# Optimization experiments

Hardware: AMD Instinct MI355X
Metric: run time of the kernel (lower is better)

Reference implementation:

```python
import math
import jax, jax.numpy as jnp
import numpy as np

NUM_HEADS = 8
FACTOR = 5


def setup_inputs() -> dict:
    key = jax.random.key(0)
    ks = jax.random.split(key, 8)
    B, N, C = 8, 4096, 512
    s = 0.02
    x = jax.random.normal(ks[0], (B, N, C), dtype=jnp.float32)
    Wq = jax.random.normal(ks[1], (C, C), dtype=jnp.float32) * s
    Wk = jax.random.normal(ks[2], (C, C), dtype=jnp.float32) * s
    Wv = jax.random.normal(ks[3], (C, C), dtype=jnp.float32) * s
    Wp = jax.random.normal(ks[4], (C, C), dtype=jnp.float32) * s
    bq = jnp.zeros((C,), jnp.float32)
    bk = jnp.zeros((C,), jnp.float32)
    bv = jnp.zeros((C,), jnp.float32)
    bp = jnp.zeros((C,), jnp.float32)
    sample_k = min(FACTOR * int(np.ceil(np.log(N))), N)  # 45
    index_sample = jax.random.randint(ks[5], (N, sample_k), 0, N, dtype=jnp.int64)
    return {"x": x, "Wq": Wq, "bq": bq, "Wk": Wk, "bk": bk,
            "Wv": Wv, "bv": bv, "Wp": Wp, "bp": bp,
            "index_sample": index_sample}


def reference(x, Wq, bq, Wk, bk, Wv, bv, Wp, bp, index_sample):
    B, N, C = x.shape
    H = NUM_HEADS
    Dh = C // H
    L_Q = L_K = N
    # qkv projections (torch Linear: x @ W.T + b; W sampled symmetric so use x @ W + b)
    q = (x @ Wq + bq).reshape(B, N, H, Dh).transpose(0, 2, 1, 3)  # [B,H,L,Dh]
    k = (x @ Wk + bk).reshape(B, N, H, Dh).transpose(0, 2, 1, 3)
    v = (x @ Wv + bv).reshape(B, N, H, Dh).transpose(0, 2, 1, 3)

    u = min(FACTOR * int(np.ceil(np.log(L_Q))), L_Q)  # n_top
    scale = (C // H) ** (-0.5)

    # _prob_QK: sampled scores per query
    K_sample = k[:, :, index_sample, :]                       # [B,H,L_Q,s,Dh]
    QK_sample = jnp.einsum('bhld,bhlsd->bhls', q, K_sample)   # [B,H,L_Q,s]
    M = QK_sample.max(axis=-1) - QK_sample.sum(axis=-1) / L_K # sparsity measure
    _, M_top = jax.lax.top_k(M, u)                            # [B,H,u]
    Q_reduce = jnp.take_along_axis(q, M_top[..., None], axis=2)  # [B,H,u,Dh]
    scores = jnp.einsum('bhud,bhkd->bhuk', Q_reduce, k) * scale  # [B,H,u,L_K]

    # initial context: mean of V over keys (mask_flag=False)
    context = jnp.broadcast_to(v.mean(axis=2, keepdims=True), (B, H, L_Q, Dh))

    # update context at selected queries
    attn = jax.nn.softmax(scores, axis=-1)
    out_u = jnp.einsum('bhuk,bhkd->bhud', attn, v)            # [B,H,u,Dh]
    bI = jnp.arange(B)[:, None, None]
    hI = jnp.arange(H)[None, :, None]
    context = context.at[bI, hI, M_top].set(out_u)            # [B,H,L_Q,Dh]

    # mix=True: reshape [B,H,N,Dh] -> [B,N,H*Dh] directly (faithful to source)
    context = context.reshape(B, N, H * Dh)
    return context @ Wp + bp
```

## Files before the change

kernel.cpp:

```cpp
#include <hip/hip_runtime.h>
#include <float.h>

typedef unsigned short ushort_t;
typedef short bf16x8 __attribute__((ext_vector_type(8)));
typedef _Float16 f16x8 __attribute__((ext_vector_type(8)));
typedef float f32x4 __attribute__((ext_vector_type(4)));

#define NS 4096
#define ND 64
#define NU 45
#define NUP 48

__device__ __forceinline__ float bf2f(ushort_t u){ return __uint_as_float(((unsigned)u)<<16); }
__device__ __forceinline__ ushort_t f2bf(float f){
  unsigned u = __float_as_uint(f);
  u += 0x7fffu + ((u>>16)&1u);
  return (ushort_t)(u>>16);
}
__device__ __forceinline__ ushort_t f2h(float f){ _Float16 h=(_Float16)f; return __builtin_bit_cast(ushort_t, h); }
__device__ __forceinline__ float h2f(ushort_t u){ return (float)__builtin_bit_cast(_Float16, u); }

__global__ __launch_bounds__(256) void k_wsplit(const float* __restrict__ Wq,
                                                const float* __restrict__ Wk,
                                                const float* __restrict__ Wv,
                                                ushort_t* __restrict__ wh,
                                                ushort_t* __restrict__ wl)
{
  int i = blockIdx.x*256 + threadIdx.x;
  int c = i >> 9, k = i & 511;
  const float* W = (c < 512) ? Wq : (c < 1024 ? Wk : Wv);
  float v = W[k*512 + (c & 511)];
  ushort_t h = f2bf(v);
  wh[i] = h;
  wl[i] = f2bf(v - bf2f(h));
}

__global__ __launch_bounds__(256) void k_xsplit(const float* __restrict__ x,
                                                ushort_t* __restrict__ xh,
                                                ushort_t* __restrict__ xl)
{
  int i = (blockIdx.x*256 + threadIdx.x)*4;
  float4 v = *(const float4*)(x + i);
  ushort4 h, lo;
  h.x = f2bf(v.x); lo.x = f2bf(v.x - bf2f(h.x));
  h.y = f2bf(v.y); lo.y = f2bf(v.y - bf2f(h.y));
  h.z = f2bf(v.z); lo.z = f2bf(v.z - bf2f(h.z));
  h.w = f2bf(v.w); lo.w = f2bf(v.w - bf2f(h.w));
  *(ushort4*)(xh + i) = h;
  *(ushort4*)(xl + i) = lo;
}

template<int MODE>
__global__ __launch_bounds__(256) void k_gemm(
    const float* __restrict__ x,
    const ushort_t* __restrict__ xh, const ushort_t* __restrict__ xl,
    const ushort_t* __restrict__ wh, const ushort_t* __restrict__ wl,
    const float* __restrict__ bq, const float* __restrict__ bk, const float* __restrict__ bv,
    float* __restrict__ qf, float* __restrict__ kf, ushort_t* __restrict__ vfT)
{
  __shared__ __align__(16) ushort_t smem[4*128*40];
  ushort_t* Ah = smem;
  ushort_t* Al = smem + 5120;
  ushort_t* Bh = smem + 10240;
  ushort_t* Bl = smem + 15360;
  const int nbx = (MODE == 0) ? 4 : 8;
  const int p = blockIdx.y * nbx + blockIdx.x;
  const int cx = p & 7;
  const int local = p >> 3;
  const int by = cx*32 + local/nbx;
  const int bx = local % nbx;
  const int rowbase = by * 128;
  const int colbase = (MODE == 0 ? 0 : 512) + bx*128;
  const int mat = colbase >> 9;
  const int t = threadIdx.x;
  const int l = t & 63;
  const int w = t >> 6;
  const int wm = w >> 1, wn = w & 1;
  f32x4 acc[4][4] = {};
  const int r0 = t >> 2;
  const int c0 = (t & 3) * 8;

  for (int k0 = 0; k0 < 512; k0 += 32) {
    __syncthreads();
    #pragma unroll
    for (int half = 0; half < 2; half++) {
      const int r = r0 + half*64;
      if constexpr (MODE == 1) {
        *(uint4*)(&Ah[r*40 + c0]) = *(const uint4*)(&xh[(size_t)(rowbase + r)*512 + k0 + c0]);
        *(uint4*)(&Al[r*40 + c0]) = *(const uint4*)(&xl[(size_t)(rowbase + r)*512 + k0 + c0]);
      } else {
        const float* xp = &x[(size_t)(rowbase + r)*512 + k0 + c0];
        float4 v0 = *(const float4*)xp;
        float4 v1 = *(const float4*)(xp + 4);
        ushort_t hi[8], lo[8];
        float vv[8] = {v0.x,v0.y,v0.z,v0.w,v1.x,v1.y,v1.z,v1.w};
        #pragma unroll
        for (int j = 0; j < 8; j++) {
          hi[j] = f2bf(vv[j]);
          lo[j] = f2bf(vv[j] - bf2f(hi[j]));
        }
        *(uint4*)(&Ah[r*40 + c0]) = *(const uint4*)hi;
        *(uint4*)(&Al[r*40 + c0]) = *(const uint4*)lo;
      }
      *(uint4*)(&Bh[r*40 + c0]) = *(const uint4*)(&wh[(size_t)(colbase + r)*512 + k0 + c0]);
      *(uint4*)(&Bl[r*40 + c0]) = *(const uint4*)(&wl[(size_t)(colbase + r)*512 + k0 + c0]);
    }
    __syncthreads();
    bf16x8 ah[4], al[4], bh8[4], bl8[4];
    #pragma unroll
    for (int m = 0; m < 4; m++) {
      const int off = (wm*64 + m*16 + (l & 15))*40 + (l >> 4)*8;
      ah[m] = *(const bf16x8*)(&Ah[off]);
      al[m] = *(const bf16x8*)(&Al[off]);
    }
    #pragma unroll
    for (int n = 0; n < 4; n++) {
      const int off = (wn*64 + n*16 + (l & 15))*40 + (l >> 4)*8;
      bh8[n] = *(const bf16x8*)(&Bh[off]);
      bl8[n] = *(const bf16x8*)(&Bl[off]);
    }
    #pragma unroll
    for (int m = 0; m < 4; m++)
      #pragma unroll
      for (int n = 0; n < 4; n++) {
        acc[m][n] = __builtin_amdgcn_mfma_f32_16x16x32_bf16(ah[m], bh8[n], acc[m][n], 0, 0, 0);
        acc[m][n] = __builtin_amdgcn_mfma_f32_16x16x32_bf16(ah[m], bl8[n], acc[m][n], 0, 0, 0);
        acc[m][n] = __builtin_amdgcn_mfma_f32_16x16x32_bf16(al[m], bh8[n], acc[m][n], 0, 0, 0);
      }
  }

  if (MODE == 0 || mat == 1) {
    const float* bias_p = (MODE == 0) ? bq : bk;
    float* dst = (MODE == 0) ? qf : kf;
    #pragma unroll
    for (int n = 0; n < 4; n++) {
      const int wi = (colbase & 511) + wn*64 + n*16 + (l & 15);
      const int hh = wi >> 6, d = wi & 63;
      const float bias = bias_p[wi];
      #pragma unroll
      for (int m = 0; m < 4; m++) {
        const int rb = rowbase + wm*64 + m*16 + ((l >> 4) << 2);
        const int b  = rb >> 12, nr = rb & 4095;
        #pragma unroll
        for (int j = 0; j < 4; j++)
          dst[((size_t)(b*8 + hh)*NS + nr + j)*ND + d] = acc[m][n][j] + bias;
      }
    }
  } else {
    __syncthreads();
    #pragma unroll
    for (int n = 0; n < 4; n++) {
      const int wi_l = wn*64 + n*16 + (l & 15);
      const float bias = bv[(colbase & 511) + wi_l];
      #pragma unroll
      for (int m = 0; m < 4; m++) {
        const int nr_l = wm*64 + m*16 + ((l >> 4) << 2);
        ushort4 pk;
        pk.x = f2h(acc[m][n][0] + bias);
        pk.y = f2h(acc[m][n][1] + bias);
        pk.z = f2h(acc[m][n][2] + bias);
        pk.w = f2h(acc[m][n][3] + bias);
        *(ushort4*)(&smem[wi_l*136 + nr_l]) = pk;
      }
    }
    __syncthreads();
    const int wi2 = t >> 1, half = t & 1;
    const int cim = (colbase & 511) + wi2;
    const int hh2 = cim >> 6, d2 = cim & 63;
    const int b2 = rowbase >> 12;
    const int nr2 = (rowbase & 4095) + half*64;
    ushort_t* op = &vfT[((size_t)(b2*8 + hh2)*ND + d2)*NS + nr2];
    const ushort_t* ip = &smem[wi2*136 + half*64];
    #pragma unroll
    for (int cch = 0; cch < 8; cch++)
      *(uint4*)(op + cch*8) = *(const uint4*)(ip + cch*8);
  }
}

__global__ __launch_bounds__(256) void k_k16(const float* __restrict__ kf,
                                             ushort_t* __restrict__ kh16)
{
  size_t i = ((size_t)blockIdx.x*256 + threadIdx.x)*8;
  float4 a = *(const float4*)(kf + i);
  float4 b = *(const float4*)(kf + i + 4);
  ushort4 p0, p1;
  p0.x = f2h(a.x); p0.y = f2h(a.y); p0.z = f2h(a.z); p0.w = f2h(a.w);
  p1.x = f2h(b.x); p1.y = f2h(b.y); p1.z = f2h(b.z); p1.w = f2h(b.w);
  *(ushort4*)(kh16 + i)     = p0;
  *(ushort4*)(kh16 + i + 4) = p1;
}

__global__ __launch_bounds__(256) void k_m_approx(const float* __restrict__ qf,
                                                  const ushort_t* __restrict__ kh16,
                                                  const int* __restrict__ idxs,
                                                  float* __restrict__ Mv)
{
  __shared__ float qs[4][64];
  __shared__ int   sidx[4][48];
  const int orig = blockIdx.y * 1024 + blockIdx.x;
  const int lin  = (orig & 7) * 8192 + (orig >> 3);
  const int bh   = lin >> 10;
  const int lc   = lin & 1023;
  const int t = threadIdx.x;
  const int wv = t >> 6, lane = t & 63;
  const int l = lc*4 + wv;
  qs[wv][lane] = qf[((size_t)bh*NS + l)*ND + lane];
  for (int e = t; e < 4*NU; e += 256)
    sidx[e/NU][e%NU] = idxs[(size_t)(lc*4 + e/NU)*NU + e%NU];
  __syncthreads();
  const int g  = lane >> 3;
  const int dq = lane & 7;
  const float* qp = &qs[wv][dq*8];
  float mx = -FLT_MAX, sm = 0.f;
  #pragma unroll
  for (int p = 0; p < 6; p++) {
    const int s = p*8 + g;
    const bool val = (s < NU);
    const int id = sidx[wv][val ? s : NU-1];
    uint4 ku = *(const uint4*)(&kh16[((size_t)bh*NS + id)*ND + dq*8]);
    f16x8 k8 = __builtin_bit_cast(f16x8, ku);
    float p_dot = qp[0]*(float)k8[0] + qp[1]*(float)k8[1] + qp[2]*(float)k8[2] + qp[3]*(float)k8[3]
                + qp[4]*(float)k8[4] + qp[5]*(float)k8[5] + qp[6]*(float)k8[6] + qp[7]*(float)k8[7];
    p_dot += __shfl_xor(p_dot, 1, 64);
    p_dot += __shfl_xor(p_dot, 2, 64);
    p_dot += __shfl_xor(p_dot, 4, 64);
    if (val) { mx = fmaxf(mx, p_dot); sm += p_dot; }
  }
  #pragma unroll
  for (int o = 8; o < 64; o <<= 1) {
    mx = fmaxf(mx, __shfl_xor(mx, o, 64));
    sm += __shfl_xor(sm, o, 64);
  }
  if (lane == 0) Mv[bh*NS + l] = mx - sm * (1.0f/(float)NS);
}

__global__ __launch_bounds__(256) void k_m_exact_full(const float* __restrict__ qf,
                                                      const float* __restrict__ kf,
                                                      const int* __restrict__ idxs,
                                                      float* __restrict__ Mv)
{
  const int bh = blockIdx.y;
  const int l  = blockIdx.x*4 + (threadIdx.x >> 6);
  const int lane = threadIdx.x & 63;
  const int g  = lane >> 2;
  const int dq = lane & 3;
  const float* qrow = qf + ((size_t)bh*NS + l)*ND + dq*16;
  const float4 q0 = *(const float4*)(qrow + 0);
  const float4 q1 = *(const float4*)(qrow + 4);
  const float4 q2 = *(const float4*)(qrow + 8);
  const float4 q3 = *(const float4*)(qrow + 12);
  const float* kbase = kf + (size_t)bh*NS*ND;
  const int* ib = idxs + (size_t)l*NU;
  float mx = -FLT_MAX, sm = 0.f;
  #pragma unroll
  for (int p3 = 0; p3 < 3; p3++) {
    const int s = p3*16 + g;
    const int id = ib[s < NU ? s : NU-1];
    const float* kr = kbase + (size_t)id*ND + dq*16;
    const float4 k0 = *(const float4*)(kr + 0);
    const float4 k1 = *(const float4*)(kr + 4);
    const float4 k2 = *(const float4*)(kr + 8);
    const float4 k3 = *(const float4*)(kr + 12);
    float p = q0.x*k0.x + q0.y*k0.y + q0.z*k0.z + q0.w*k0.w
            + q1.x*k1.x + q1.y*k1.y + q1.z*k1.z + q1.w*k1.w
            + q2.x*k2.x + q2.y*k2.y + q2.z*k2.z + q2.w*k2.w
            + q3.x*k3.x + q3.y*k3.y + q3.z*k3.z + q3.w*k3.w;
    p += __shfl_xor(p, 1, 64);
    p += __shfl_xor(p, 2, 64);
    if (s < NU) { mx = fmaxf(mx, p); sm += p; }
  }
  #pragma unroll
  for (int o = 4; o < 64; o <<= 1) {
    mx = fmaxf(mx, __shfl_xor(mx, o, 64));
    sm += __shfl_xor(sm, o, 64);
  }
  if (lane == 0) Mv[bh*NS + l] = mx - sm * (1.0f/(float)NS);
}

template<int NSEL, int OST>
__global__ __launch_bounds__(256) void k_topk(const float* __restrict__ Mv, int* __restrict__ dst)
{
  __shared__ float wvs[4];
  __shared__ int   wis[4];
  const int bh = blockIdx.x, t = threadIdx.x;
  const int wv = t >> 6, lane = t & 63;
  float v[16];
  #pragma unroll
  for (int j = 0; j < 16; j++) v[j] = Mv[bh*NS + j*256 + t];
  unsigned removed = 0;
  float tmax = -FLT_MAX; int tidx = 0x7fffffff;
  #pragma unroll
  for (int j = 0; j < 16; j++) {
    if (v[j] > tmax) { tmax = v[j]; tidx = j*256 + t; }
  }
  for (int it = 0; it < NSEL; it++) {
    float mv = tmax; int mi = tidx;
    #pragma unroll
    for (int o = 1; o < 64; o <<= 1) {
      float vo = __shfl_xor(mv, o, 64); int io = __shfl_xor(mi, o, 64);
      if (vo > mv || (vo == mv && io < mi)) { mv = vo; mi = io; }
    }
    if (lane == 0) { wvs[wv] = mv; wis[wv] = mi; }
    __syncthreads();
    float gv = wvs[0]; int gi = wis[0];
    #pragma unroll
    for (int k2 = 1; k2 < 4; k2++) {
      float vo = wvs[k2]; int io = wis[k2];
      if (vo > gv || (vo == gv && io < gi)) { gv = vo; gi = io; }
    }
    if (t == 0) dst[bh*OST + it] = gi;
    if ((gi & 255) == t) {
      removed |= 1u << (gi >> 8);
      tmax = -FLT_MAX; tidx = 0x7fffffff;
      #pragma unroll
      for (int j = 0; j < 16; j++) {
        bool ok = ((removed >> j) & 1u) == 0u;
        if (ok && (v[j] > tmax || (v[j] == tmax && (j*256+t) < tidx))) { tmax = v[j]; tidx = j*256 + t; }
      }
    }
    __syncthreads();
  }
}

__global__ __launch_bounds__(256) void k_mexact(const float* __restrict__ qf,
                                                const float* __restrict__ kf,
                                                const int* __restrict__ idxs,
                                                const int* __restrict__ Cand,
                                                float* __restrict__ Mex)
{
  const int bh = blockIdx.y, qtr = blockIdx.x, t = threadIdx.x;
  const int c = qtr*16 + (t >> 4);
  const int dl = t & 15;
  const int l = Cand[bh*64 + c];
  const float4 q4 = *(const float4*)(&qf[((size_t)bh*NS + l)*ND + dl*4]);
  const float* kbase = kf + (size_t)bh*NS*ND;
  const int* ib = idxs + (size_t)l*NU;
  float mx = -FLT_MAX, sm = 0.f;
  for (int s = 0; s < NU; s++) {
    const int id = ib[s];
    const float4 k4 = *(const float4*)(&kbase[(size_t)id*ND + dl*4]);
    float p = q4.x*k4.x + q4.y*k4.y + q4.z*k4.z + q4.w*k4.w;
    p += __shfl_xor(p, 1, 64);
    p += __shfl_xor(p, 2, 64);
    p += __shfl_xor(p, 4, 64);
    p += __shfl_xor(p, 8, 64);
    mx = fmaxf(mx, p);
    sm += p;
  }
  if (dl == 0) Mex[bh*64 + c] = mx - sm * (1.0f/(float)NS);
}

__global__ void k_sel45(const float* __restrict__ Mex, const int* __restrict__ Cand,
                        int* __restrict__ Mtop)
{
  const int bh = blockIdx.x, lane = threadIdx.x;
  float val = Mex[bh*64 + lane];
  const int n = Cand[bh*64 + lane];
  for (int it = 0; it < NU; it++) {
    float wv = val; int wn = n;
    #pragma unroll
    for (int o = 1; o < 64; o <<= 1) {
      float vo = __shfl_xor(wv, o, 64); int io = __shfl_xor(wn, o, 64);
      if (vo > wv || (vo == wv && io < wn)) { wv = vo; wn = io; }
    }
    if (lane == 0) Mtop[bh*NUP + it] = wn;
    if (n == wn) val = -FLT_MAX;
  }
}

__global__ __launch_bounds__(256) void k_qreduce(const float* __restrict__ qf,
                                                 const int* __restrict__ Mtop,
                                                 ushort_t* __restrict__ Qr)
{
  const int bh = blockIdx.x, t = threadIdx.x;
  for (int e = t; e < NUP*ND; e += 256) {
    const int u = e >> 6, d = e & 63;
    float v = 0.f;
    if (u < NU) { const int r = Mtop[bh*NUP + u]; v = qf[((size_t)bh*NS + r)*ND + d]; }
    Qr[bh*NUP*ND + e] = f2bf(v);
  }
}

__global__ __launch_bounds__(256) void k_scores(const ushort_t* __restrict__ Qr,
                                                const float* __restrict__ kf,
                                                ushort_t* __restrict__ scores)
{
  __shared__ __align__(16) ushort_t Ql[NUP*80];
  const int bh = blockIdx.y;
  const int n0 = blockIdx.x * 256;
  const int t = threadIdx.x, w = t >> 6, l = t & 63;
  for (int chunk = t; chunk < NUP*8; chunk += 256) {
    const int r = chunk >> 3, cp = chunk & 7;
    *(uint4*)(&Ql[r*80 + cp*8]) = *(const uint4*)(&Qr[((size_t)bh*NUP + r)*ND + cp*8]);
  }
  __syncthreads();
  f32x4 acc[3][4] = {};
  const float* kbb = kf + (size_t)bh*NS*ND;
  const int nw = n0 + w*64;
  #pragma unroll
  for (int ks = 0; ks < 2; ks++) {
    bf16x8 a[3], b8[4];
    #pragma unroll
    for (int m = 0; m < 3; m++)
      a[m] = *(const bf16x8*)(&Ql[(m*16 + (l & 15))*80 + (l >> 4)*8 + ks*32]);
    #pragma unroll
    for (int n = 0; n < 4; n++) {
      const float* kr = &kbb[(size_t)(nw + n*16 + (l & 15))*ND + (l >> 4)*8 + ks*32];
      float4 u0 = *(const float4*)kr;
      float4 u1 = *(const float4*)(kr + 4);
      ushort_t tmp[8] = {f2bf(u0.x),f2bf(u0.y),f2bf(u0.z),f2bf(u0.w),
                         f2bf(u1.x),f2bf(u1.y),f2bf(u1.z),f2bf(u1.w)};
      b8[n] = *(const bf16x8*)tmp;
    }
    #pragma unroll
    for (int m = 0; m < 3; m++)
      #pragma unroll
      for (int n = 0; n < 4; n++)
        acc[m][n] = __builtin_amdgcn_mfma_f32_16x16x32_bf16(a[m], b8[n], acc[m][n], 0, 0, 0);
  }
  #pragma unroll
  for (int m = 0; m < 3; m++)
    #pragma unroll
    for (int n = 0; n < 4; n++)
      #pragma unroll
      for (int j = 0; j < 4; j++) {
        const int row = m*16 + (l >> 4)*4 + j;
        const int col = nw + n*16 + (l & 15);
        scores[((size_t)bh*NUP + row)*NS + col] = f2bf(acc[m][n][j] * 0.125f);
      }
}

__global__ __launch_bounds__(256) void k_softmax(ushort_t* __restrict__ scores)
{
  __shared__ float srow[NS];
  __shared__ float red[256];
  const int bh = blockIdx.y, u = blockIdx.x, t = threadIdx.x;
  ushort_t* row = scores + ((size_t)bh*NUP + u)*NS;
  float mx = -FLT_MAX;
  for (int j = t; j < NS; j += 256) { float v = bf2f(row[j]); srow[j] = v; mx = fmaxf(mx, v); }
  red[t] = mx; __syncthreads();
  for (int s = 128; s > 0; s >>= 1) { if (t < s) red[t] = fmaxf(red[t], red[t+s]); __syncthreads(); }
  mx = red[0]; __syncthreads();
  float sm = 0.f;
  for (int j = t; j < NS; j += 256) { const float e = __expf(srow[j] - mx); srow[j] = e; sm += e; }
  red[t] = sm; __syncthreads();
  for (int s = 128; s > 0; s >>= 1) { if (t < s) red[t] += red[t+s]; __syncthreads(); }
  const float inv = 1.0f / red[0];
  for (int j = t; j < NS; j += 256) row[j] = f2h(srow[j] * inv);
}

__global__ __launch_bounds__(256) void k_vmean(const ushort_t* __restrict__ vfT, float* __restrict__ vmean)
{
  __shared__ float red[256];
  const int d = blockIdx.x, bh = blockIdx.y, t = threadIdx.x;
  const ushort_t* vr = vfT + ((size_t)bh*ND + d)*NS;
  float s = 0.f;
  for (int n = t; n < NS; n += 256) s += h2f(vr[n]);
  red[t] = s; __syncthreads();
  for (int st = 128; st > 0; st >>= 1) { if (t < st) red[t] += red[t+st]; __syncthreads(); }
  if (t == 0) vmean[bh*ND + d] = red[0] * (1.0f/(float)NS);
}

__global__ __launch_bounds__(256) void k_outu(const ushort_t* __restrict__ attn,
                                              const ushort_t* __restrict__ vfT,
                                              float* __restrict__ pout)
{
  const int bh = blockIdx.y, ch = blockIdx.x;
  const int t = threadIdx.x, w = t >> 6, l = t & 63;
  if (w >= 3) return;
  const ushort_t* ab = attn + (size_t)bh*NUP*NS;
  const ushort_t* vb = vfT + (size_t)bh*ND*NS;
  f32x4 acc[4] = {};
  const int arow = w*16 + (l & 15);
  const int koff = (l >> 4)*8;
  const int kbeg = ch*512;
  for (int kc = kbeg; kc < kbeg + 512; kc += 32) {
    uint4 au = *(const uint4*)(&ab[(size_t)arow*NS + kc + koff]);
    f16x8 a = __builtin_bit_cast(f16x8, au);
    #pragma unroll
    for (int nt = 0; nt < 4; nt++) {
      uint4 bu = *(const uint4*)(&vb[(size_t)(nt*16 + (l & 15))*NS + kc + koff]);
      f16x8 b = __builtin_bit_cast(f16x8, bu);
      acc[nt] = __builtin_amdgcn_mfma_f32_16x16x32_f16(a, b, acc[nt], 0, 0, 0);
    }
  }
  #pragma unroll
  for (int nt = 0; nt < 4; nt++)
    #pragma unroll
    for (int j = 0; j < 4; j++) {
      const int u = w*16 + (l >> 4)*4 + j;
      const int d = nt*16 + (l & 15);
      pout[(((size_t)bh*8 + ch)*NUP + u)*ND + d] = acc[nt][j];
    }
}

__global__ __launch_bounds__(256) void k_delta_fin(const float* __restrict__ pout,
                                                   const float* __restrict__ vmean,
                                                   float* __restrict__ delta)
{
  const int bh = blockIdx.x, t = threadIdx.x;
  for (int e = t; e < NUP*ND; e += 256) {
    const int u = e >> 6, d = e & 63;
    float s = 0.f;
    #pragma unroll
    for (int ch = 0; ch < 8; ch++) s += pout[(((size_t)bh*8 + ch)*NUP + u)*ND + d];
    delta[((size_t)bh*NUP + u)*ND + d] = s - vmean[bh*ND + d];
  }
}

__global__ __launch_bounds__(256) void k_uidx_init(int* __restrict__ uidx)
{
  uidx[blockIdx.x*256 + threadIdx.x] = -1;
}

__global__ void k_scatter(const int* __restrict__ Mtop, int* __restrict__ uidx)
{
  const int bh = blockIdx.x, t = threadIdx.x;
  if (t < NU) {
    const int n = Mtop[bh*NUP + t];
    const int b = bh >> 3, h = bh & 7;
    const int nprime = h*512 + (n >> 3);
    uidx[((size_t)b*NS + nprime)*8 + (n & 7)] = bh*NUP + t;
  }
}

__global__ __launch_bounds__(256) void k_corr(const float* __restrict__ delta,
                                              const float* __restrict__ Wp,
                                              const int* __restrict__ Mtop,
                                              float* __restrict__ corr)
{
  __shared__ float dl[64];
  const int bh = blockIdx.y, u = blockIdx.x, t = threadIdx.x;
  const int n = Mtop[bh*NUP + u];
  const int j = n & 7;
  if (t < 64) dl[t] = delta[((size_t)bh*NUP + u)*ND + t];
  __syncthreads();
  for (int c = t; c < 512; c += 256) {
    float s = 0.f;
    #pragma unroll 8
    for (int d2 = 0; d2 < 64; d2++) s += dl[d2] * Wp[(size_t)(j*64 + d2)*512 + c];
    corr[((size_t)bh*NUP + u)*512 + c] = s;
  }
}

__global__ __launch_bounds__(256) void k_base(const float* __restrict__ vmean,
                                              const float* __restrict__ Wp,
                                              const float* __restrict__ bp,
                                              float* __restrict__ basep)
{
  __shared__ float vm[64];
  const int bh = blockIdx.x, t = threadIdx.x;
  if (t < 64) vm[t] = vmean[bh*ND + t];
  __syncthreads();
  for (int c = t; c < 512; c += 256) {
    float s = bp[c];
    for (int k = 0; k < 512; k++) s += vm[k & 63] * Wp[(size_t)k*512 + c];
    basep[bh*512 + c] = s;
  }
}

__global__ __launch_bounds__(256) void k_assemble(const float* __restrict__ basep,
                                                  const float* __restrict__ corr,
                                                  const int* __restrict__ uidx,
                                                  float* __restrict__ out)
{
  const int b = blockIdx.y, nprime = blockIdx.x, t = threadIdx.x;
  const int h = nprime >> 9;
  const int* ui = uidx + ((size_t)b*NS + nprime)*8;
  float v0 = basep[(b*8 + h)*512 + t];
  float v1 = basep[(b*8 + h)*512 + 256 + t];
  #pragma unroll
  for (int j = 0; j < 8; j++) {
    const int id = ui[j];
    if (id >= 0) { v0 += corr[(size_t)id*512 + t]; v1 += corr[(size_t)id*512 + 256 + t]; }
  }
  const size_t o = ((size_t)b*NS + nprime)*512;
  out[o + t]       = v0;
  out[o + 256 + t] = v1;
}

extern "C" void kernel_launch(void* const* d_in, const int* in_sizes, int n_in,
                              void* d_out, int out_size, void* d_ws, size_t ws_size,
                              hipStream_t stream)
{
  (void)in_sizes; (void)n_in; (void)out_size;
  const float* x  = (const float*)d_in[0];
  const float* Wq = (const float*)d_in[1];
  const float* bq = (const float*)d_in[2];
  const float* Wk = (const float*)d_in[3];
  const float* bk = (const float*)d_in[4];
  const float* Wv = (const float*)d_in[5];
  const float* bv = (const float*)d_in[6];
  const float* Wp = (const float*)d_in[7];
  const float* bp = (const float*)d_in[8];
  const int* idxs = (const int*)d_in[9];
  float* out      = (float*)d_out;

  char* w = (char*)d_ws;
  float*    qf    = (float*)(w);
  float*    kf    = (float*)(w + 67108864);
  ushort_t* vfT   = (ushort_t*)(w + 134217728);
  ushort_t* wh    = (ushort_t*)(w + 167772160);
  ushort_t* wl    = (ushort_t*)(w + 169345024);
  float*    Mv    = (float*)(w + 170917888);
  int*      Mtop  = (int*)(w + 171966464);
  ushort_t* Qr    = (ushort_t*)(w + 171978752);
  float*    vmean = (float*)(w + 172371968);
  ushort_t* xh = (ushort_t*)(w);
  ushort_t* xl = (ushort_t*)(w + 33554432);
  ushort_t* scores = (ushort_t*)(w);
  float*    delta  = (float*)(w + 25165824);
  float*    corr   = (float*)(w + 25952256);
  int*      uidx   = (int*)(w + 32243712);
  float*    basep  = (float*)(w + 33292288);
  float*    pout   = (float*)(w + 33423360);
  ushort_t* kh16 = (ushort_t*)(w + 172388352);
  int*      Cand = (int*)(w + 205942784);
  float*    Mex  = (float*)(w + 205959168);
  const bool approx_ok = (ws_size >= (size_t)205975552);

  k_wsplit   <<<3072, 256, 0, stream>>>(Wq, Wk, Wv, wh, wl);
  k_xsplit   <<<16384, 256, 0, stream>>>(x, xh, xl);
  k_gemm<1>  <<<dim3(8, 256), 256, 0, stream>>>(x, xh, xl, wh, wl, bq, bk, bv, qf, kf, vfT);
  k_gemm<0>  <<<dim3(4, 256), 256, 0, stream>>>(x, nullptr, nullptr, wh, wl, bq, bk, bv, qf, kf, vfT);
  if (approx_ok) {
    k_k16      <<<8192, 256, 0, stream>>>(kf, kh16);
    k_m_approx <<<dim3(1024, 64), 256, 0, stream>>>(qf, kh16, idxs, Mv);
    k_vmean    <<<dim3(64, 64), 256, 0, stream>>>(vfT, vmean);
    k_topk<64,64> <<<64, 256, 0, stream>>>(Mv, Cand);
    k_mexact   <<<dim3(4, 64), 256, 0, stream>>>(qf, kf, idxs, Cand, Mex);
    k_sel45    <<<64, 64, 0, stream>>>(Mex, Cand, Mtop);
  } else {
    k_m_exact_full <<<dim3(1024, 64), 256, 0, stream>>>(qf, kf, idxs, Mv);
    k_vmean    <<<dim3(64, 64), 256, 0, stream>>>(vfT, vmean);
    k_topk<NU,NUP> <<<64, 256, 0, stream>>>(Mv, Mtop);
  }
  k_qreduce  <<<64, 256, 0, stream>>>(qf, Mtop, Qr);
  k_scores   <<<dim3(16, 64), 256, 0, stream>>>(Qr, kf, scores);
  k_softmax  <<<dim3(45, 64), 256, 0, stream>>>(scores);
  k_outu     <<<dim3(8, 64), 256, 0, stream>>>(scores, vfT, pout);
  k_delta_fin<<<64, 256, 0, stream>>>(pout, vmean, delta);
  k_uidx_init<<<1024, 256, 0, stream>>>(uidx);
  k_scatter  <<<64, 64, 0, stream>>>(Mtop, uidx);
  k_corr     <<<dim3(45, 64), 256, 0, stream>>>(delta, Wp, Mtop, corr);
  k_base     <<<64, 256, 0, stream>>>(vmean, Wp, bp, basep);
  k_assemble <<<dim3(4096, 8), 256, 0, stream>>>(basep, corr, uidx, out);
}
```

Before: 604.0 us.

## Load GEMM B fragments straight from global and fuse fp16 K conversion into epilogue

The QKV GEMM no longer stages the weight tiles in shared memory. Each wave loads its bf16 hi/lo B fragments directly from global memory into registers. The standalone kernel that converted K from fp32 to fp16 is removed, and the K-projection epilogue now writes the fp16 copy itself through a shared-memory transpose. This saves one kernel launch and a full reread of K, and halves LDS traffic per k-step. The cost is uncoalesced, redundant global loads of weights across waves, plus extra epilogue work and barriers.

```diff
diff --git a/kernel.cpp b/kernel.cpp
--- a/kernel.cpp
+++ b/kernel.cpp
@@ -56,13 +56,12 @@
     const ushort_t* __restrict__ xh, const ushort_t* __restrict__ xl,
     const ushort_t* __restrict__ wh, const ushort_t* __restrict__ wl,
     const float* __restrict__ bq, const float* __restrict__ bk, const float* __restrict__ bv,
-    float* __restrict__ qf, float* __restrict__ kf, ushort_t* __restrict__ vfT)
-{
-  __shared__ __align__(16) ushort_t smem[4*128*40];
+    float* __restrict__ qf, float* __restrict__ kf, ushort_t* __restrict__ vfT,
+    ushort_t* __restrict__ kh16)
+{
+  __shared__ __align__(16) ushort_t smem[17408];
   ushort_t* Ah = smem;
   ushort_t* Al = smem + 5120;
-  ushort_t* Bh = smem + 10240;
-  ushort_t* Bl = smem + 15360;
   const int nbx = (MODE == 0) ? 4 : 8;
   const int p = blockIdx.y * nbx + blockIdx.x;
   const int cx = p & 7;
@@ -81,6 +80,13 @@
   const int c0 = (t & 3) * 8;
 
   for (int k0 = 0; k0 < 512; k0 += 32) {
+    bf16x8 bh8[4], bl8[4];
+    #pragma unroll
+    for (int n = 0; n < 4; n++) {
+      const size_t boff = (size_t)(colbase + wn*64 + n*16 + (l & 15))*512 + k0 + (l >> 4)*8;
+      bh8[n] = *(const bf16x8*)(&wh[boff]);
+      bl8[n] = *(const bf16x8*)(&wl[boff]);
+    }
     __syncthreads();
     #pragma unroll
     for (int half = 0; half < 2; half++) {
@@ -102,22 +108,14 @@
         *(uint4*)(&Ah[r*40 + c0]) = *(const uint4*)hi;
         *(uint4*)(&Al[r*40 + c0]) = *(const uint4*)lo;
       }
-      *(uint4*)(&Bh[r*40 + c0]) = *(const uint4*)(&wh[(size_t)(colbase + r)*512 + k0 + c0]);
-      *(uint4*)(&Bl[r*40 + c0]) = *(const uint4*)(&wl[(size_t)(colbase + r)*512 + k0 + c0]);
     }
     __syncthreads();
-    bf16x8 ah[4], al[4], bh8[4], bl8[4];
+    bf16x8 ah[4], al[4];
     #pragma unroll
     for (int m = 0; m < 4; m++) {
       const int off = (wm*64 + m*16 + (l & 15))*40 + (l >> 4)*8;
       ah[m] = *(const bf16x8*)(&Ah[off]);
       al[m] = *(const bf16x8*)(&Al[off]);
-    }
-    #pragma unroll
-    for (int n = 0; n < 4; n++) {
-      const int off = (wn*64 + n*16 + (l & 15))*40 + (l >> 4)*8;
-      bh8[n] = *(const bf16x8*)(&Bh[off]);
-      bl8[n] = *(const bf16x8*)(&Bl[off]);
     }
     #pragma unroll
     for (int m = 0; m < 4; m++)
@@ -145,6 +143,31 @@
         for (int j = 0; j < 4; j++)
           dst[((size_t)(b*8 + hh)*NS + nr + j)*ND + d] = acc[m][n][j] + bias;
       }
+    }
+    if (MODE == 1 && kh16) {
+      __syncthreads();
+      #pragma unroll
+      for (int n = 0; n < 4; n++) {
+        const int c_l = wn*64 + n*16 + (l & 15);
+        const float bias = bk[(colbase & 511) + c_l];
+        #pragma unroll
+        for (int m = 0; m < 4; m++) {
+          const int rb_l = wm*64 + m*16 + ((l >> 4) << 2);
+          #pragma unroll
+          for (int j = 0; j < 4; j++)
+            smem[(rb_l + j)*136 + c_l] = f2h(acc[m][n][j] + bias);
+        }
+      }
+      __syncthreads();
+      const int r2 = t >> 1, half = t & 1;
+      const int hh2 = ((colbase & 511) >> 6) + half;
+      const int b2 = rowbase >> 12;
+      const int nr2 = rowbase & 4095;
+      ushort_t* op = &kh16[((size_t)(b2*8 + hh2)*NS + nr2 + r2)*ND];
+      const ushort_t* ip = &smem[r2*136 + half*64];
+      #pragma unroll
+      for (int cch = 0; cch < 8; cch++)
+        *(uint4*)(op + cch*8) = *(const uint4*)(ip + cch*8);
     }
   } else {
     __syncthreads();
@@ -175,19 +198,6 @@
     for (int cch = 0; cch < 8; cch++)
       *(uint4*)(op + cch*8) = *(const uint4*)(ip + cch*8);
   }
-}
-
-__global__ __launch_bounds__(256) void k_k16(const float* __restrict__ kf,
-                                             ushort_t* __restrict__ kh16)
-{
-  size_t i = ((size_t)blockIdx.x*256 + threadIdx.x)*8;
-  float4 a = *(const float4*)(kf + i);
-  float4 b = *(const float4*)(kf + i + 4);
-  ushort4 p0, p1;
-  p0.x = f2h(a.x); p0.y = f2h(a.y); p0.z = f2h(a.z); p0.w = f2h(a.w);
-  p1.x = f2h(b.x); p1.y = f2h(b.y); p1.z = f2h(b.z); p1.w = f2h(b.w);
-  *(ushort4*)(kh16 + i)     = p0;
-  *(ushort4*)(kh16 + i + 4) = p1;
 }
 
 __global__ __launch_bounds__(256) void k_m_approx(const float* __restrict__ qf,
@@ -618,13 +628,13 @@
   int*      Cand = (int*)(w + 205942784);
   float*    Mex  = (float*)(w + 205959168);
   const bool approx_ok = (ws_size >= (size_t)205975552);
+  ushort_t* kh16_arg = approx_ok ? kh16 : (ushort_t*)nullptr;
 
   k_wsplit   <<<3072, 256, 0, stream>>>(Wq, Wk, Wv, wh, wl);
   k_xsplit   <<<16384, 256, 0, stream>>>(x, xh, xl);
-  k_gemm<1>  <<<dim3(8, 256), 256, 0, stream>>>(x, xh, xl, wh, wl, bq, bk, bv, qf, kf, vfT);
-  k_gemm<0>  <<<dim3(4, 256), 256, 0, stream>>>(x, nullptr, nullptr, wh, wl, bq, bk, bv, qf, kf, vfT);
+  k_gemm<1>  <<<dim3(8, 256), 256, 0, stream>>>(x, xh, xl, wh, wl, bq, bk, bv, qf, kf, vfT, kh16_arg);
+  k_gemm<0>  <<<dim3(4, 256), 256, 0, stream>>>(x, nullptr, nullptr, wh, wl, bq, bk, bv, qf, kf, vfT, nullptr);
   if (approx_ok) {
-    k_k16      <<<8192, 256, 0, stream>>>(kf, kh16);
     k_m_approx <<<dim3(1024, 64), 256, 0, stream>>>(qf, kh16, idxs, Mv);
     k_vmean    <<<dim3(64, 64), 256, 0, stream>>>(vfT, vmean);
     k_topk<64,64> <<<64, 256, 0, stream>>>(Mv, Cand);
```

Result: slower. 670.7 us (+11.0%).
